# Performance work log

Hardware: AMD Instinct MI355X
Metric: run time of the kernel (lower is better)

Reference implementation:

```python
import jax, jax.numpy as jnp
import numpy as np

B, NX, NY, E, H, L = 4, 1024, 1024, 512, 8, 4
DH = E // H
FF = 4 * E
SCALE = DH ** (-0.5)
EPS = 1e-5


def _ln(x, g, b):
    mu = jnp.mean(x, axis=-1, keepdims=True)
    var = jnp.mean((x - mu) ** 2, axis=-1, keepdims=True)
    return (x - mu) * jax.lax.rsqrt(var + EPS) * g + b


def setup_inputs() -> dict:
    key = jax.random.key(0)
    ks = jax.random.split(key, 16)
    s = 0.02
    inp = {
        'x': jax.random.normal(ks[0], (B, NX, E), jnp.float32),
        'y': jax.random.normal(ks[1], (B, NY, E), jnp.float32),
        'x_mask': jax.random.randint(ks[2], (B, NX), 0, 2, jnp.int32),
        'y_mask': jax.random.randint(ks[3], (B, NY), 0, 2, jnp.int32),
        # stacked per-layer params (L leading dim)
        'Wq': jax.random.normal(ks[4], (L, E, E), jnp.float32) * s,
        'bq': jnp.zeros((L, E), jnp.float32),
        'Wk': jax.random.normal(ks[5], (L, E, E), jnp.float32) * s,
        'bk': jnp.zeros((L, E), jnp.float32),
        'Wv': jax.random.normal(ks[6], (L, E, E), jnp.float32) * s,
        'bv': jnp.zeros((L, E), jnp.float32),
        'Wo': jax.random.normal(ks[7], (L, E, E), jnp.float32) * s,
        'bo': jnp.zeros((L, E), jnp.float32),
        'g1': jnp.ones((L, E), jnp.float32),
        'be1': jnp.zeros((L, E), jnp.float32),
        'g2': jnp.ones((L, E), jnp.float32),
        'be2': jnp.zeros((L, E), jnp.float32),
        'W1': jax.random.normal(ks[8], (L, E, FF), jnp.float32) * s,
        'bf1': jnp.zeros((L, FF), jnp.float32),
        'W2': jax.random.normal(ks[9], (L, FF, E), jnp.float32) * s,
        'bf2': jnp.zeros((L, E), jnp.float32),
    }
    return inp


def _forward(x, y, mask4, Wq, bq, Wk, bk, Wv, bv, Wo, bo, g1, be1, g2, be2, W1, bf1, W2, bf2):
    # mask4: (B,1,NX,NY) int, 0 = masked
    attn_prev = None
    out = x
    for l in range(L):
        q = x @ Wq[l] + bq[l]              # (B,NX,E)
        k = y @ Wk[l] + bk[l]
        v = y @ Wv[l] + bv[l]
        # faithful non-standard head split: plain reshape, no transpose
        q = q.reshape(B, H, NX, DH)
        k = k.reshape(B, H, NY, DH)
        v = v.reshape(B, H, NY, DH)
        scores = jnp.einsum('bhnd,bhmd->bhnm', q, k) * SCALE
        scores = jnp.where(mask4 == 0, jnp.float32(-1e9), scores)
        a = jax.nn.softmax(scores, axis=-1)
        if attn_prev is not None:
            a = a + attn_prev  # residual attention
        attn_prev = a
        o = jnp.einsum('bhnm,bhmd->bhnd', a, v)
        o = jnp.transpose(o, (0, 2, 1, 3)).reshape(B, NX, E)
        o = o @ Wo[l] + bo[l]
        h = _ln(x + o, g1[l], be1[l])
        ff = jax.nn.gelu(h @ W1[l] + bf1[l], approximate=False) @ W2[l] + bf2[l]
        out = _ln(h + ff, g2[l], be2[l])
        # NOTE: faithful to source, x and y are NOT updated between layers;
        # only the attention residual chains. Final output is last layer's out.
    return out


def reference(x, y, x_mask, y_mask, Wq, bq, Wk, bk, Wv, bv, Wo, bo, g1, be1, g2, be2, W1, bf1, W2, bf2):
    mask4 = (x_mask[:, :, None].astype(jnp.float32) @ y_mask[:, None, :].astype(jnp.float32)).astype(jnp.int32)[:, None]
    return _forward(x, y, mask4, Wq, bq, Wk, bk, Wv, bv, Wo, bo, g1, be1, g2, be2, W1, bf1, W2, bf2)
```

## Files before the change

kernel.cpp:

```cpp
#include <hip/hip_runtime.h>
#include <cstdint>

using u16    = unsigned short;
using u32    = unsigned int;
using bf16x8 = __attribute__((ext_vector_type(8))) __bf16;
using f32x4  = __attribute__((ext_vector_type(4))) float;

__device__ __forceinline__ u16 f2bf(float f) {
    u32 u = __builtin_bit_cast(u32, f);
    u += 0x7FFFu + ((u >> 16) & 1u);
    return (u16)(u >> 16);
}
__device__ __forceinline__ float bf2f(u16 u) {
    return __builtin_bit_cast(float, (u32)u << 16);
}
__device__ __forceinline__ u32 pk_bf16(float a, float b) {
    u32 r;
    asm("v_cvt_pk_bf16_f32 %0, %1, %2" : "=v"(r) : "v"(a), "v"(b));
    return r;
}
__device__ __forceinline__ float hw_exp2(float x) {
    float r;
    asm("v_exp_f32 %0, %1" : "=v"(r) : "v"(x));
    return r;
}
__device__ __forceinline__ void load_lds16(const u16* g, u16* l) {
    __builtin_amdgcn_global_load_lds((const __attribute__((address_space(1))) void*)g,
                                     (__attribute__((address_space(3))) void*)l, 16, 0, 0);
}

__global__ __launch_bounds__(256) void cvt2_kernel(const float* __restrict__ a,
                                                   const float* __restrict__ b,
                                                   u16* __restrict__ oa,
                                                   u16* __restrict__ ob)
{
    const int bid = blockIdx.x;
    const float* in = bid < 2048 ? a : b;
    u16* out = bid < 2048 ? oa : ob;
    int i = ((bid & 2047) * 256 + threadIdx.x) * 4;
    float4 v = *(const float4*)(in + i);
    uint2 o;
    o.x = (u32)f2bf(v.x) | ((u32)f2bf(v.y) << 16);
    o.y = (u32)f2bf(v.z) | ((u32)f2bf(v.w) << 16);
    *(uint2*)(out + i) = o;
}

__global__ __launch_bounds__(256) void wtrans_kernel(const float* __restrict__ Wq,
                                                     const float* __restrict__ Wk,
                                                     const float* __restrict__ Wv,
                                                     const float* __restrict__ Wo,
                                                     const float* __restrict__ W1,
                                                     const float* __restrict__ W2,
                                                     u16* __restrict__ wt)
{
    const int gid = blockIdx.x;
    const float* src; u16* dst; int K = 512, N = 512; int n0, k0;
    if (gid < 2560) {
        int z = gid >> 8, tid = gid & 255;
        switch (z) {
            case 0: case 1: case 2: case 3:
                src = Wq + (size_t)z * 262144;        dst = wt + (size_t)z * 262144;            break;
            case 4: case 5: case 6: case 7:
                src = Wk + (size_t)(z - 4) * 262144;  dst = wt + 1048576 + (size_t)(z - 4) * 262144; break;
            case 8: src = Wv + 3 * 262144;  dst = wt + 2097152; break;
            default: src = Wo + 3 * 262144; dst = wt + 2359296; break;
        }
        n0 = (tid & 15) * 32; k0 = (tid >> 4) * 32;
    } else if (gid < 3584) {
        int tid = gid - 2560;
        src = W1 + 3 * 1048576; dst = wt + 2621440; K = 512; N = 2048;
        n0 = (tid & 63) * 32; k0 = (tid >> 6) * 32;
    } else {
        int tid = gid - 3584;
        src = W2 + 3 * 1048576; dst = wt + 3670016; K = 2048; N = 512;
        n0 = (tid & 15) * 32; k0 = (tid >> 4) * 32;
    }
    __shared__ float tile[32][33];
    int tx = threadIdx.x, ty = threadIdx.y;
    #pragma unroll
    for (int i = 0; i < 4; i++) {
        int r = ty + i * 8;
        tile[r][tx] = src[(size_t)(k0 + r) * N + n0 + tx];
    }
    __syncthreads();
    #pragma unroll
    for (int i = 0; i < 4; i++) {
        int rn = ty + i * 8;
        dst[(size_t)(n0 + rn) * K + k0 + tx] = f2bf(tile[tx][rn]);
    }
}

template<int BNF>
__device__ __forceinline__ void gemm_core32(const u16* __restrict__ A,
                                            const u16* __restrict__ BT,
                                            int K, int m0, int n0,
                                            u16 (*As)[32], u16 (*Bs)[32],
                                            f32x4 acc[4][BNF])
{
    const int t    = threadIdx.x;
    const int lane = t & 63, wid = t >> 6;
    const int wm = wid >> 1, wn = wid & 1;
    const int lrow = lane & 15, kg = lane >> 4;
    const int sr = lane >> 2;
    const int sg = ((lane & 3) ^ ((lane >> 3) & 3)) * 8;

    auto stage = [&](int buf, int ks) {
        #pragma unroll
        for (int i = 0; i < 2; i++) {
            int row = wid * 32 + i * 16;
            load_lds16(&A[(size_t)(m0 + row + sr) * K + ks + sg], &As[buf * 128 + row][0]);
        }
        if constexpr (BNF == 4) {
            #pragma unroll
            for (int i = 0; i < 2; i++) {
                int row = wid * 32 + i * 16;
                load_lds16(&BT[(size_t)(n0 + row + sr) * K + ks + sg], &Bs[buf * 128 + row][0]);
            }
        } else {
            int row = wid * 16;
            load_lds16(&BT[(size_t)(n0 + row + sr) * K + ks + sg], &Bs[buf * 64 + row][0]);
        }
    };

    stage(0, 0);
    __syncthreads();
    int buf = 0;
    for (int ks = 0; ks < K; ks += 32) {
        if (ks + 32 < K) stage(buf ^ 1, ks + 32);
        const int rg = (kg ^ ((lrow >> 1) & 3)) * 8;
        bf16x8 af[4], bfv[BNF];
        #pragma unroll
        for (int i = 0; i < 4; i++)
            af[i] = *(const bf16x8*)&As[buf * 128 + wm * 64 + i * 16 + lrow][rg];
        #pragma unroll
        for (int j = 0; j < BNF; j++)
            bfv[j] = *(const bf16x8*)&Bs[buf * (BNF * 32) + wn * (BNF * 16) + j * 16 + lrow][rg];
        #pragma unroll
        for (int i = 0; i < 4; i++)
            #pragma unroll
            for (int j = 0; j < BNF; j++)
                acc[i][j] = __builtin_amdgcn_mfma_f32_16x16x32_bf16(af[i], bfv[j], acc[i][j], 0, 0, 0);
        __syncthreads();
        buf ^= 1;
    }
}

__global__ __launch_bounds__(256) void qkv_gemm_kernel(const u16* __restrict__ x16,
                                                       const u16* __restrict__ y16,
                                                       const u16* __restrict__ wt,
                                                       u16* __restrict__ qkv,
                                                       const float* __restrict__ bq,
                                                       const float* __restrict__ bk,
                                                       const float* __restrict__ bv,
                                                       const int* __restrict__ x_mask)
{
    __shared__ u16 As[256][32];
    __shared__ u16 Bs[256][32];
    const int z = blockIdx.z;
    const u16* A; const u16* BT; const float* bias;
    if (z < 4)      { A = x16; BT = wt + (size_t)z * 262144;                 bias = bq + z * 512; }
    else if (z < 8) { A = y16; BT = wt + 1048576 + (size_t)(z - 4) * 262144; bias = bk + (z - 4) * 512; }
    else            { A = y16; BT = wt + 2097152;                            bias = bv + 3 * 512; }
    u16* out = qkv + (size_t)z * 2097152;

    const int m0 = blockIdx.y * 128, n0 = blockIdx.x * 128;
    f32x4 acc[4][4];
    #pragma unroll
    for (int i = 0; i < 4; i++)
        #pragma unroll
        for (int j = 0; j < 4; j++) acc[i][j] = f32x4{0.f, 0.f, 0.f, 0.f};
    gemm_core32<4>(A, BT, 512, m0, n0, As, Bs, acc);

    const int lane = threadIdx.x & 63, wid = threadIdx.x >> 6;
    const int wm = wid >> 1, wn = wid & 1;
    const int lrow = lane & 15, kg = lane >> 4;
    #pragma unroll
    for (int i = 0; i < 4; i++)
        #pragma unroll
        for (int j = 0; j < 4; j++)
            #pragma unroll
            for (int r = 0; r < 4; r++) {
                int row = m0 + wm * 64 + i * 16 + kg * 4 + r;
                int col = n0 + wn * 64 + j * 16 + lrow;
                float v = acc[i][j][r] + bias[col];
                if (z < 4) v *= 0.180336880f * (x_mask[row] ? 1.f : 0.f);
                out[(size_t)row * 512 + col] = f2bf(v);
            }
}

template<int BNF, int EPI>
__global__ __launch_bounds__(256) void gemm_bt_kernel(const u16* __restrict__ A,
                                                      const u16* __restrict__ BT,
                                                      const float* __restrict__ bias,
                                                      void* __restrict__ outp,
                                                      const float* __restrict__ res,
                                                      int N, int K)
{
    __shared__ u16 As[256][32];
    __shared__ u16 Bs[BNF * 64][32];
    const int m0 = blockIdx.y * 128, n0 = blockIdx.x * (BNF * 32);
    f32x4 acc[4][BNF];
    #pragma unroll
    for (int i = 0; i < 4; i++)
        #pragma unroll
        for (int j = 0; j < BNF; j++) acc[i][j] = f32x4{0.f, 0.f, 0.f, 0.f};
    gemm_core32<BNF>(A, BT, K, m0, n0, As, Bs, acc);

    const int lane = threadIdx.x & 63, wid = threadIdx.x >> 6;
    const int wm = wid >> 1, wn = wid & 1;
    const int lrow = lane & 15, kg = lane >> 4;
    #pragma unroll
    for (int i = 0; i < 4; i++)
        #pragma unroll
        for (int j = 0; j < BNF; j++)
            #pragma unroll
            for (int r = 0; r < 4; r++) {
                int row = m0 + wm * 64 + i * 16 + kg * 4 + r;
                int col = n0 + wn * (BNF * 16) + j * 16 + lrow;
                float v = acc[i][j][r] + bias[col];
                if constexpr (EPI == 1) {
                    ((float*)outp)[(size_t)row * N + col] = v + res[(size_t)row * N + col];
                } else {
                    v = 0.5f * v * (1.f + erff(v * 0.70710678118654752f));
                    ((u16*)outp)[(size_t)row * N + col] = f2bf(v);
                }
            }
}

__global__ __launch_bounds__(256) void vtrans_kernel(const u16* __restrict__ v, u16* __restrict__ vt)
{
    const int bh = blockIdx.y, m0 = blockIdx.x * 64;
    const int b = bh >> 3, h = bh & 7;
    const u16* src = v + (size_t)b * 524288 + (size_t)h * 65536;
    u16* dst = vt + (size_t)bh * 65536;
    __shared__ u16 tile[64][72];
    const int t = threadIdx.x;
    #pragma unroll
    for (int i = 0; i < 2; i++) {
        int idx = t + i * 256, r = idx >> 3, q = idx & 7;
        *(uint4*)&tile[r][q * 8] = *(const uint4*)&src[(size_t)(m0 + r) * 64 + q * 8];
    }
    __syncthreads();
    #pragma unroll
    for (int i = 0; i < 2; i++) {
        int idx = t + i * 256, d = idx >> 3, q = idx & 7;
        alignas(16) u16 tmp[8];
        #pragma unroll
        for (int j = 0; j < 8; j++) tmp[j] = tile[q * 8 + j][d];
        *(uint4*)&dst[(size_t)d * 1024 + m0 + q * 8] = *(uint4*)tmp;
    }
}

__global__ __launch_bounds__(512) void attn_kernel(const u16* __restrict__ qkv,
                                                   const int* __restrict__ x_mask,
                                                   const int* __restrict__ y_mask,
                                                   const u16* __restrict__ vt,
                                                   u16* __restrict__ obuf)
{
    __shared__ __align__(16) char smem[65536];
    u16 (*Kb)[4][32][64] = reinterpret_cast<u16(*)[4][32][64]>(smem);
    u16 (*Vb)[64][32]    = reinterpret_cast<u16(*)[64][32]>(smem + 32768);
    float* ymb           = reinterpret_cast<float*>(smem + 40960);
    u16 (*Ps)[32][40]    = reinterpret_cast<u16(*)[32][40]>(smem + 45056);
    u16 (*Osh)[32][72]   = reinterpret_cast<u16(*)[32][72]>(smem);

    const int t = threadIdx.x;
    const int wid = t >> 6, lane = t & 63;
    const int lrow = lane & 15, kg = lane >> 4;
    const int L  = wid & 3;
    const int qh = wid >> 2;

    const int gid  = blockIdx.x;
    const int orig = (gid & 7) * 64 + (gid >> 3);
    const int bh = orig >> 4, qt = orig & 15;
    const int b = bh >> 3, h = bh & 7;
    const int q0 = qt * 64;

    const size_t headoff = (size_t)b * 524288 + (size_t)h * 65536;
    const u16* Q  = qkv + (size_t)L * 2097152 + headoff;
    const u16* VT = vt + (size_t)bh * 65536;

    for (int i = t; i < 1024; i += 512)
        ymb[i] = y_mask[b * 1024 + i] ? 0.f : -1e9f;

    const int kscol = ((lane & 7) ^ (lane >> 3)) * 8;
    const int vsrow = wid * 16 + (lane >> 2);
    const int vscol = (((lane & 3) ^ ((vsrow & 3) ^ ((vsrow >> 2) & 3))) * 8);
    const int fswz  = (lrow & 3) ^ ((lrow >> 2) & 3);

    const int fr0 = wid * 8 + (lane >> 3);
    const int fr1 = 64 + fr0;
    const u16* ksrc0 = qkv + (size_t)(4 + (fr0 >> 5)) * 2097152 + headoff + (size_t)(fr0 & 31) * 64 + kscol;
    const u16* ksrc1 = qkv + (size_t)(4 + (fr1 >> 5)) * 2097152 + headoff + (size_t)(fr1 & 31) * 64 + kscol;
    const u16* vsrc  = VT + (size_t)vsrow * 1024 + vscol;

    auto stage_load = [&](int mt, uint4& k0r, uint4& k1r, uint4& vr) {
        const int m0 = mt * 32;
        k0r = *(const uint4*)(ksrc0 + (size_t)m0 * 64);
        k1r = *(const uint4*)(ksrc1 + (size_t)m0 * 64);
        if (wid < 4) vr = *(const uint4*)(vsrc + m0);
    };
    auto stage_write = [&](int buf, const uint4& k0r, const uint4& k1r, const uint4& vr) {
        u16* kbase = &Kb[buf][0][0][0];
        *(uint4*)(kbase + (0 * 512 + wid * 64) * 8 + lane * 8) = k0r;
        *(uint4*)(kbase + (1 * 512 + wid * 64) * 8 + lane * 8) = k1r;
        if (wid < 4)
            *(uint4*)(&Vb[buf][wid * 16][0] + lane * 8) = vr;
    };

    bf16x8 aq[2][2];
    #pragma unroll
    for (int i = 0; i < 2; i++) {
        const int qr = q0 + qh * 32 + i * 16 + lrow;
        aq[i][0] = *(const bf16x8*)&Q[(size_t)qr * 64 + kg * 8];
        aq[i][1] = *(const bf16x8*)&Q[(size_t)qr * 64 + 32 + kg * 8];
    }
    float xmf[2];
    #pragma unroll
    for (int i = 0; i < 2; i++)
        xmf[i] = x_mask[b * 1024 + q0 + qh * 32 + i * 16 + lrow] ? 1.f : 0.f;

    f32x4 oacc[2][4];
    float psum[2] = {0.f, 0.f};
    #pragma unroll
    for (int i = 0; i < 2; i++)
        #pragma unroll
        for (int d = 0; d < 4; d++) oacc[i][d] = f32x4{0.f, 0.f, 0.f, 0.f};

    uint4 k0r, k1r, vr;
    stage_load(0, k0r, k1r, vr);
    stage_write(0, k0r, k1r, vr);
    __syncthreads();

    for (int mt = 0; mt < 32; mt++) {
        const int buf = mt & 1;
        const int m0 = mt * 32;
        if (mt < 31) stage_load(mt + 1, k0r, k1r, vr);

        bf16x8 kb[2][2];
        #pragma unroll
        for (int nf = 0; nf < 2; nf++)
            #pragma unroll
            for (int kk = 0; kk < 2; kk++)
                kb[nf][kk] = *(const bf16x8*)&Kb[buf][L][nf * 16 + lrow][((kk * 4 + kg) ^ (lrow & 7)) * 8];

        float yb[2][4];
        #pragma unroll
        for (int nf = 0; nf < 2; nf++)
            #pragma unroll
            for (int r = 0; r < 4; r++) yb[nf][r] = ymb[m0 + nf * 16 + kg * 4 + r];

        #pragma unroll
        for (int i = 0; i < 2; i++) {
            f32x4 s0 = f32x4{0.f, 0.f, 0.f, 0.f}, s1 = f32x4{0.f, 0.f, 0.f, 0.f};
            s0 = __builtin_amdgcn_mfma_f32_16x16x32_bf16(kb[0][0], aq[i][0], s0, 0, 0, 0);
            s0 = __builtin_amdgcn_mfma_f32_16x16x32_bf16(kb[0][1], aq[i][1], s0, 0, 0, 0);
            s1 = __builtin_amdgcn_mfma_f32_16x16x32_bf16(kb[1][0], aq[i][0], s1, 0, 0, 0);
            s1 = __builtin_amdgcn_mfma_f32_16x16x32_bf16(kb[1][1], aq[i][1], s1, 0, 0, 0);
            float p0 = hw_exp2(fmaf(xmf[i], yb[0][0], s0[0]));
            float p1 = hw_exp2(fmaf(xmf[i], yb[0][1], s0[1]));
            float p2 = hw_exp2(fmaf(xmf[i], yb[0][2], s0[2]));
            float p3 = hw_exp2(fmaf(xmf[i], yb[0][3], s0[3]));
            float p4 = hw_exp2(fmaf(xmf[i], yb[1][0], s1[0]));
            float p5 = hw_exp2(fmaf(xmf[i], yb[1][1], s1[1]));
            float p6 = hw_exp2(fmaf(xmf[i], yb[1][2], s1[2]));
            float p7 = hw_exp2(fmaf(xmf[i], yb[1][3], s1[3]));
            psum[i] += ((p0 + p1) + (p2 + p3)) + ((p4 + p5) + (p6 + p7));
            *(u32*)&Ps[wid][i * 16 + lrow][kg * 4]          = pk_bf16(p0, p1);
            *(u32*)&Ps[wid][i * 16 + lrow][kg * 4 + 2]      = pk_bf16(p2, p3);
            *(u32*)&Ps[wid][i * 16 + lrow][16 + kg * 4]     = pk_bf16(p4, p5);
            *(u32*)&Ps[wid][i * 16 + lrow][16 + kg * 4 + 2] = pk_bf16(p6, p7);
        }

        bf16x8 pa[2], vbf[4];
        #pragma unroll
        for (int i = 0; i < 2; i++)
            pa[i] = *(const bf16x8*)&Ps[wid][i * 16 + lrow][kg * 8];
        #pragma unroll
        for (int d = 0; d < 4; d++)
            vbf[d] = *(const bf16x8*)&Vb[buf][d * 16 + lrow][(kg ^ fswz) * 8];
        #pragma unroll
        for (int i = 0; i < 2; i++)
            #pragma unroll
            for (int d = 0; d < 4; d++)
                oacc[i][d] = __builtin_amdgcn_mfma_f32_16x16x32_bf16(pa[i], vbf[d], oacc[i][d], 0, 0, 0);

        if (mt < 31) stage_write(buf ^ 1, k0r, k1r, vr);
        __syncthreads();
    }

    #pragma unroll
    for (int i = 0; i < 2; i++) {
        psum[i] += __shfl_xor(psum[i], 16);
        psum[i] += __shfl_xor(psum[i], 32);
    }
    float invr[2][4];
    #pragma unroll
    for (int i = 0; i < 2; i++) {
        float inv = 1.f / psum[i];
        #pragma unroll
        for (int r = 0; r < 4; r++) invr[i][r] = __shfl(inv, kg * 4 + r, 16);
    }

    #pragma unroll
    for (int i = 0; i < 2; i++)
        #pragma unroll
        for (int d = 0; d < 4; d++)
            #pragma unroll
            for (int r = 0; r < 4; r++)
                Osh[wid][i * 16 + kg * 4 + r][d * 16 + lrow] = f2bf(oacc[i][d][r] * invr[i][r]);
    __syncthreads();

    {
        const int row64 = t >> 3, c0 = (t & 7) * 8;
        const int wbase = (row64 >> 5) * 4, lr = row64 & 31;
        float a8[8] = {0, 0, 0, 0, 0, 0, 0, 0};
        #pragma unroll
        for (int l = 0; l < 4; l++) {
            uint4 v = *(const uint4*)&Osh[wbase + l][lr][c0];
            const u16* pv = (const u16*)&v;
            #pragma unroll
            for (int j = 0; j < 8; j++) a8[j] += bf2f(pv[j]);
        }
        alignas(16) u16 tmp[8];
        #pragma unroll
        for (int j = 0; j < 8; j++) tmp[j] = f2bf(a8[j]);
        *(uint4*)&obuf[(size_t)(b * 1024 + q0 + row64) * 512 + h * 64 + c0] = *(uint4*)tmp;
    }
}

template<int MODE>
__global__ __launch_bounds__(256) void ln_kernel(const float* __restrict__ in,
                                                 const float* __restrict__ g,
                                                 const float* __restrict__ be,
                                                 float* __restrict__ out32,
                                                 u16* __restrict__ out16)
{
    const int wid = threadIdx.x >> 6, lane = threadIdx.x & 63;
    const int row = blockIdx.x * 4 + wid;
    const float* x = in + (size_t)row * 512;
    float4 v1 = *(const float4*)&x[lane * 8];
    float4 v2 = *(const float4*)&x[lane * 8 + 4];
    float xv[8] = { v1.x, v1.y, v1.z, v1.w, v2.x, v2.y, v2.z, v2.w };
    float s = 0.f, s2 = 0.f;
    #pragma unroll
    for (int j = 0; j < 8; j++) { s += xv[j]; s2 += xv[j] * xv[j]; }
    #pragma unroll
    for (int off = 32; off > 0; off >>= 1) {
        s  += __shfl_xor(s, off, 64);
        s2 += __shfl_xor(s2, off, 64);
    }
    const float mean = s * (1.f / 512.f);
    const float var  = s2 * (1.f / 512.f) - mean * mean;
    const float rstd = rsqrtf(var + 1e-5f);
    float ov[8];
    #pragma unroll
    for (int j = 0; j < 8; j++) {
        int col = lane * 8 + j;
        ov[j] = (xv[j] - mean) * rstd * g[col] + be[col];
    }
    *(float4*)&out32[(size_t)row * 512 + lane * 8]     = float4{ ov[0], ov[1], ov[2], ov[3] };
    *(float4*)&out32[(size_t)row * 512 + lane * 8 + 4] = float4{ ov[4], ov[5], ov[6], ov[7] };
    if constexpr (MODE == 0) {
        alignas(16) u16 tmp[8];
        #pragma unroll
        for (int j = 0; j < 8; j++) tmp[j] = f2bf(ov[j]);
        *(uint4*)&out16[(size_t)row * 512 + lane * 8] = *(uint4*)tmp;
    }
}

extern "C" void kernel_launch(void* const* d_in, const int* in_sizes, int n_in,
                              void* d_out, int out_size, void* d_ws, size_t ws_size,
                              hipStream_t stream) {
    const float* x      = (const float*)d_in[0];
    const float* y      = (const float*)d_in[1];
    const int*   x_mask = (const int*)d_in[2];
    const int*   y_mask = (const int*)d_in[3];
    const float* Wq  = (const float*)d_in[4];
    const float* bq  = (const float*)d_in[5];
    const float* Wk  = (const float*)d_in[6];
    const float* bk  = (const float*)d_in[7];
    const float* Wv  = (const float*)d_in[8];
    const float* bv  = (const float*)d_in[9];
    const float* Wo  = (const float*)d_in[10];
    const float* bo  = (const float*)d_in[11];
    const float* g1  = (const float*)d_in[12];
    const float* be1 = (const float*)d_in[13];
    const float* g2  = (const float*)d_in[14];
    const float* be2 = (const float*)d_in[15];
    const float* W1  = (const float*)d_in[16];
    const float* bf1 = (const float*)d_in[17];
    const float* W2  = (const float*)d_in[18];
    const float* bf2 = (const float*)d_in[19];

    char* p = (char*)d_ws;
    auto alloc = [&](size_t bytes) { char* r = p; p += (bytes + 255) & ~(size_t)255; return r; };
    u16*   x16   = (u16*)alloc(2097152ULL * 2);
    u16*   y16   = (u16*)alloc(2097152ULL * 2);
    u16*   wt    = (u16*)alloc(4718592ULL * 2);
    u16*   qkv   = (u16*)alloc(9ULL * 2097152 * 2);
    u16*   vt    = (u16*)alloc(2097152ULL * 2);
    u16*   obuf  = (u16*)alloc(2097152ULL * 2);
    float* xo    = (float*)alloc(2097152ULL * 4);
    float* h32   = (float*)alloc(2097152ULL * 4);
    u16*   h16   = (u16*)alloc(2097152ULL * 2);
    u16*   ffmid = (u16*)alloc(8388608ULL * 2);
    float* ffout = (float*)alloc(2097152ULL * 4);
    if ((size_t)(p - (char*)d_ws) > ws_size) return;

    cvt2_kernel<<<4096, 256, 0, stream>>>(x, y, x16, y16);
    wtrans_kernel<<<4608, dim3(32, 8), 0, stream>>>(Wq, Wk, Wv, Wo, W1, W2, wt);
    qkv_gemm_kernel<<<dim3(4, 32, 9), 256, 0, stream>>>(x16, y16, wt, qkv, bq, bk, bv, x_mask);
    vtrans_kernel<<<dim3(16, 32), 256, 0, stream>>>(qkv + 8ULL * 2097152, vt);
    attn_kernel<<<512, 512, 0, stream>>>(qkv, x_mask, y_mask, vt, obuf);
    gemm_bt_kernel<2, 1><<<dim3(8, 32), 256, 0, stream>>>(obuf, wt + 2359296, bo + 3 * 512, xo, x, 512, 512);
    ln_kernel<0><<<1024, 256, 0, stream>>>(xo, g1 + 3 * 512, be1 + 3 * 512, h32, h16);
    gemm_bt_kernel<4, 2><<<dim3(16, 32), 256, 0, stream>>>(h16, wt + 2621440, bf1 + 3 * 2048, ffmid, nullptr, 2048, 512);
    gemm_bt_kernel<2, 1><<<dim3(8, 32), 256, 0, stream>>>(ffmid, wt + 3670016, bf2 + 3 * 512, ffout, h32, 512, 2048);
    ln_kernel<1><<<1024, 256, 0, stream>>>(ffout, g2 + 3 * 512, be2 + 3 * 512, (float*)d_out, nullptr);
}
```

Baseline: 174.1 us.

## Split-K the output and FFN-down GEMMs into two partials summed in LayerNorm

The Wo projection and the second FFN GEMM now run as a split-K over two halves (grid z=2), and each half writes an fp32 partial to its own buffer. The LayerNorm kernel reads both partials plus the residual and sums them, which removes the residual add from the GEMM epilogue. The aim is to double the block count for these small-N GEMMs (256 to 512 blocks) so the GPU is better occupied. The cost is an extra fp32 partial write and read through memory.

```diff
diff --git a/kernel.cpp b/kernel.cpp
--- a/kernel.cpp
+++ b/kernel.cpp
@@ -93,7 +93,7 @@
 template<int BNF>
 __device__ __forceinline__ void gemm_core32(const u16* __restrict__ A,
                                             const u16* __restrict__ BT,
-                                            int K, int m0, int n0,
+                                            int Kloop, int lda, int m0, int n0,
                                             u16 (*As)[32], u16 (*Bs)[32],
                                             f32x4 acc[4][BNF])
 {
@@ -108,25 +108,25 @@
         #pragma unroll
         for (int i = 0; i < 2; i++) {
             int row = wid * 32 + i * 16;
-            load_lds16(&A[(size_t)(m0 + row + sr) * K + ks + sg], &As[buf * 128 + row][0]);
+            load_lds16(&A[(size_t)(m0 + row + sr) * lda + ks + sg], &As[buf * 128 + row][0]);
         }
         if constexpr (BNF == 4) {
             #pragma unroll
             for (int i = 0; i < 2; i++) {
                 int row = wid * 32 + i * 16;
-                load_lds16(&BT[(size_t)(n0 + row + sr) * K + ks + sg], &Bs[buf * 128 + row][0]);
+                load_lds16(&BT[(size_t)(n0 + row + sr) * lda + ks + sg], &Bs[buf * 128 + row][0]);
             }
         } else {
             int row = wid * 16;
-            load_lds16(&BT[(size_t)(n0 + row + sr) * K + ks + sg], &Bs[buf * 64 + row][0]);
+            load_lds16(&BT[(size_t)(n0 + row + sr) * lda + ks + sg], &Bs[buf * 64 + row][0]);
         }
     };
 
     stage(0, 0);
     __syncthreads();
     int buf = 0;
-    for (int ks = 0; ks < K; ks += 32) {
-        if (ks + 32 < K) stage(buf ^ 1, ks + 32);
+    for (int ks = 0; ks < Kloop; ks += 32) {
+        if (ks + 32 < Kloop) stage(buf ^ 1, ks + 32);
         const int rg = (kg ^ ((lrow >> 1) & 3)) * 8;
         bf16x8 af[4], bfv[BNF];
         #pragma unroll
@@ -169,7 +169,7 @@
     for (int i = 0; i < 4; i++)
         #pragma unroll
         for (int j = 0; j < 4; j++) acc[i][j] = f32x4{0.f, 0.f, 0.f, 0.f};
-    gemm_core32<4>(A, BT, 512, m0, n0, As, Bs, acc);
+    gemm_core32<4>(A, BT, 512, 512, m0, n0, As, Bs, acc);
 
     const int lane = threadIdx.x & 63, wid = threadIdx.x >> 6;
     const int wm = wid >> 1, wn = wid & 1;
@@ -188,23 +188,21 @@
             }
 }
 
-template<int BNF, int EPI>
-__global__ __launch_bounds__(256) void gemm_bt_kernel(const u16* __restrict__ A,
-                                                      const u16* __restrict__ BT,
-                                                      const float* __restrict__ bias,
-                                                      void* __restrict__ outp,
-                                                      const float* __restrict__ res,
-                                                      int N, int K)
+__global__ __launch_bounds__(256) void gemm_gelu_kernel(const u16* __restrict__ A,
+                                                        const u16* __restrict__ BT,
+                                                        const float* __restrict__ bias,
+                                                        u16* __restrict__ outp,
+                                                        int N, int K)
 {
     __shared__ u16 As[256][32];
-    __shared__ u16 Bs[BNF * 64][32];
-    const int m0 = blockIdx.y * 128, n0 = blockIdx.x * (BNF * 32);
-    f32x4 acc[4][BNF];
+    __shared__ u16 Bs[256][32];
+    const int m0 = blockIdx.y * 128, n0 = blockIdx.x * 128;
+    f32x4 acc[4][4];
     #pragma unroll
     for (int i = 0; i < 4; i++)
         #pragma unroll
-        for (int j = 0; j < BNF; j++) acc[i][j] = f32x4{0.f, 0.f, 0.f, 0.f};
-    gemm_core32<BNF>(A, BT, K, m0, n0, As, Bs, acc);
+        for (int j = 0; j < 4; j++) acc[i][j] = f32x4{0.f, 0.f, 0.f, 0.f};
+    gemm_core32<4>(A, BT, K, K, m0, n0, As, Bs, acc);
 
     const int lane = threadIdx.x & 63, wid = threadIdx.x >> 6;
     const int wm = wid >> 1, wn = wid & 1;
@@ -212,18 +210,51 @@
     #pragma unroll
     for (int i = 0; i < 4; i++)
         #pragma unroll
-        for (int j = 0; j < BNF; j++)
+        for (int j = 0; j < 4; j++)
             #pragma unroll
             for (int r = 0; r < 4; r++) {
                 int row = m0 + wm * 64 + i * 16 + kg * 4 + r;
-                int col = n0 + wn * (BNF * 16) + j * 16 + lrow;
+                int col = n0 + wn * 64 + j * 16 + lrow;
                 float v = acc[i][j][r] + bias[col];
-                if constexpr (EPI == 1) {
-                    ((float*)outp)[(size_t)row * N + col] = v + res[(size_t)row * N + col];
-                } else {
-                    v = 0.5f * v * (1.f + erff(v * 0.70710678118654752f));
-                    ((u16*)outp)[(size_t)row * N + col] = f2bf(v);
-                }
+                v = 0.5f * v * (1.f + erff(v * 0.70710678118654752f));
+                outp[(size_t)row * N + col] = f2bf(v);
+            }
+}
+
+__global__ __launch_bounds__(256) void gemm_part_kernel(const u16* __restrict__ A,
+                                                        const u16* __restrict__ BT,
+                                                        const float* __restrict__ bias,
+                                                        float* __restrict__ outA,
+                                                        float* __restrict__ outB,
+                                                        int N, int Kstride, int Khalf)
+{
+    __shared__ u16 As[256][32];
+    __shared__ u16 Bs[128][32];
+    const int z = blockIdx.z;
+    const int k_off = z * Khalf;
+    float* out = z == 0 ? outA : outB;
+    const int m0 = blockIdx.y * 128, n0 = blockIdx.x * 64;
+    f32x4 acc[4][2];
+    #pragma unroll
+    for (int i = 0; i < 4; i++)
+        #pragma unroll
+        for (int j = 0; j < 2; j++) acc[i][j] = f32x4{0.f, 0.f, 0.f, 0.f};
+    gemm_core32<2>(A + k_off, BT + k_off, Khalf, Kstride, m0, n0, As, Bs, acc);
+
+    const int lane = threadIdx.x & 63, wid = threadIdx.x >> 6;
+    const int wm = wid >> 1, wn = wid & 1;
+    const int lrow = lane & 15, kg = lane >> 4;
+    #pragma unroll
+    for (int i = 0; i < 4; i++)
+        #pragma unroll
+        for (int j = 0; j < 2; j++)
+            #pragma unroll
+            for (int r = 0; r < 4; r++) {
+                int row = m0 + wm * 64 + i * 16 + kg * 4 + r;
+                int col = n0 + wn * 32 + j * 16 + lrow;
+                float v = acc[i][j][r];
+                if (z == 0) v += bias[col];
+                out[(size_t)row * N + col] = v;
             }
 }
 
@@ -430,18 +461,22 @@
 }
 
 template<int MODE>
-__global__ __launch_bounds__(256) void ln_kernel(const float* __restrict__ in,
-                                                 const float* __restrict__ g,
-                                                 const float* __restrict__ be,
-                                                 float* __restrict__ out32,
-                                                 u16* __restrict__ out16)
+__global__ __launch_bounds__(256) void ln3_kernel(const float* __restrict__ ina,
+                                                  const float* __restrict__ inb,
+                                                  const float* __restrict__ inc,
+                                                  const float* __restrict__ g,
+                                                  const float* __restrict__ be,
+                                                  float* __restrict__ out32,
+                                                  u16* __restrict__ out16)
 {
     const int wid = threadIdx.x >> 6, lane = threadIdx.x & 63;
     const int row = blockIdx.x * 4 + wid;
-    const float* x = in + (size_t)row * 512;
-    float4 v1 = *(const float4*)&x[lane * 8];
-    float4 v2 = *(const float4*)&x[lane * 8 + 4];
-    float xv[8] = { v1.x, v1.y, v1.z, v1.w, v2.x, v2.y, v2.z, v2.w };
+    const size_t base = (size_t)row * 512 + lane * 8;
+    float4 a1 = *(const float4*)&ina[base],     a2 = *(const float4*)&ina[base + 4];
+    float4 b1 = *(const float4*)&inb[base],     b2 = *(const float4*)&inb[base + 4];
+    float4 c1 = *(const float4*)&inc[base],     c2 = *(const float4*)&inc[base + 4];
+    float xv[8] = { a1.x + b1.x + c1.x, a1.y + b1.y + c1.y, a1.z + b1.z + c1.z, a1.w + b1.w + c1.w,
+                    a2.x + b2.x + c2.x, a2.y + b2.y + c2.y, a2.z + b2.z + c2.z, a2.w + b2.w + c2.w };
     float s = 0.f, s2 = 0.f;
     #pragma unroll
     for (int j = 0; j < 8; j++) { s += xv[j]; s2 += xv[j] * xv[j]; }
@@ -459,13 +494,13 @@
         int col = lane * 8 + j;
         ov[j] = (xv[j] - mean) * rstd * g[col] + be[col];
     }
-    *(float4*)&out32[(size_t)row * 512 + lane * 8]     = float4{ ov[0], ov[1], ov[2], ov[3] };
-    *(float4*)&out32[(size_t)row * 512 + lane * 8 + 4] = float4{ ov[4], ov[5], ov[6], ov[7] };
+    *(float4*)&out32[base]     = float4{ ov[0], ov[1], ov[2], ov[3] };
+    *(float4*)&out32[base + 4] = float4{ ov[4], ov[5], ov[6], ov[7] };
     if constexpr (MODE == 0) {
         alignas(16) u16 tmp[8];
         #pragma unroll
         for (int j = 0; j < 8; j++) tmp[j] = f2bf(ov[j]);
-        *(uint4*)&out16[(size_t)row * 512 + lane * 8] = *(uint4*)tmp;
+        *(uint4*)&out16[base] = *(uint4*)tmp;
     }
 }
 
@@ -501,11 +536,11 @@
     u16*   qkv   = (u16*)alloc(9ULL * 2097152 * 2);
     u16*   vt    = (u16*)alloc(2097152ULL * 2);
     u16*   obuf  = (u16*)alloc(2097152ULL * 2);
-    float* xo    = (float*)alloc(2097152ULL * 4);
+    float* parA  = (float*)alloc(2097152ULL * 4);
+    float* parB  = (float*)alloc(2097152ULL * 4);
     float* h32   = (float*)alloc(2097152ULL * 4);
     u16*   h16   = (u16*)alloc(2097152ULL * 2);
     u16*   ffmid = (u16*)alloc(8388608ULL * 2);
-    float* ffout = (float*)alloc(2097152ULL * 4);
     if ((size_t)(p - (char*)d_ws) > ws_size) return;
 
     cvt2_kernel<<<4096, 256, 0, stream>>>(x, y, x16, y16);
@@ -513,9 +548,9 @@
     qkv_gemm_kernel<<<dim3(4, 32, 9), 256, 0, stream>>>(x16, y16, wt, qkv, bq, bk, bv, x_mask);
     vtrans_kernel<<<dim3(16, 32), 256, 0, stream>>>(qkv + 8ULL * 2097152, vt);
     attn_kernel<<<512, 512, 0, stream>>>(qkv, x_mask, y_mask, vt, obuf);
-    gemm_bt_kernel<2, 1><<<dim3(8, 32), 256, 0, stream>>>(obuf, wt + 2359296, bo + 3 * 512, xo, x, 512, 512);
-    ln_kernel<0><<<1024, 256, 0, stream>>>(xo, g1 + 3 * 512, be1 + 3 * 512, h32, h16);
-    gemm_bt_kernel<4, 2><<<dim3(16, 32), 256, 0, stream>>>(h16, wt + 2621440, bf1 + 3 * 2048, ffmid, nullptr, 2048, 512);
-    gemm_bt_kernel<2, 1><<<dim3(8, 32), 256, 0, stream>>>(ffmid, wt + 3670016, bf2 + 3 * 512, ffout, h32, 512, 2048);
-    ln_kernel<1><<<1024, 256, 0, stream>>>(ffout, g2 + 3 * 512, be2 + 3 * 512, (float*)d_out, nullptr);
-}
+    gemm_part_kernel<<<dim3(8, 32, 2), 256, 0, stream>>>(obuf, wt + 2359296, bo + 3 * 512, parA, parB, 512, 512, 256);
+    ln3_kernel<0><<<1024, 256, 0, stream>>>(parA, parB, x, g1 + 3 * 512, be1 + 3 * 512, h32, h16);
+    gemm_gelu_kernel<<<dim3(16, 32), 256, 0, stream>>>(h16, wt + 2621440, bf1 + 3 * 2048, ffmid, 2048, 512);
+    gemm_part_kernel<<<dim3(8, 32, 2), 256, 0, stream>>>(ffmid, wt + 3670016, bf2 + 3 * 512, parA, parB, 512, 2048, 1024);
+    ln3_kernel<1><<<1024, 256, 0, stream>>>(parA, parB, h32, g2 + 3 * 512, be2 + 3 * 512, (float*)d_out, nullptr);
+}
```

Measured after the change: 180.3 us, median of 2. +3.5%, slower.
